# Kernel tuning notes

Hardware: AMD Instinct MI355X
Metric: run time of the kernel (lower is better)

The kernel has to match this reference:

```python
import jax, jax.numpy as jnp
import numpy as np

DIM = 64
HALF = DIM // 2
K = 8
B = 3.0
HID = 256
N = 65536
MIN_BW = 1e-3
MIN_BH = 1e-3
MIN_D = 1e-3


def _mlp(x, w0, b0, w1, b1, w2, b2):
    h = jnp.tanh(x @ w0 + b0)
    h = jnp.tanh(h @ w1 + b1)
    return h @ w2 + b2


def _unconstrained_rqs(x, uW, uH, uD, tail_bound):
    # x: [N, d]; uW, uH: [N, d, K]; uD: [N, d, K-1]
    # Faithful to Durkan/Karpathy unconstrained_RQS (forward, inverse=False).
    left, right, bottom, top = -tail_bound, tail_bound, -tail_bound, tail_bound
    inside = (x >= -tail_bound) & (x <= tail_bound)

    const = float(np.log(np.exp(1.0 - MIN_D) - 1.0))
    uD = jnp.pad(uD, ((0, 0), (0, 0), (1, 1)), constant_values=const)  # [N,d,K+1]

    widths = jax.nn.softmax(uW, axis=-1)
    widths = MIN_BW + (1.0 - MIN_BW * K) * widths
    cumw = jnp.cumsum(widths, axis=-1)
    cumw = jnp.pad(cumw, ((0, 0), (0, 0), (1, 0)))
    cumw = (right - left) * cumw + left
    cumw = cumw.at[..., 0].set(left).at[..., -1].set(right)
    widths = cumw[..., 1:] - cumw[..., :-1]

    derivs = MIN_D + jax.nn.softplus(uD)  # [N,d,K+1]

    heights = jax.nn.softmax(uH, axis=-1)
    heights = MIN_BH + (1.0 - MIN_BH * K) * heights
    cumh = jnp.cumsum(heights, axis=-1)
    cumh = jnp.pad(cumh, ((0, 0), (0, 0), (1, 0)))
    cumh = (top - bottom) * cumh + bottom
    cumh = cumh.at[..., 0].set(bottom).at[..., -1].set(top)
    heights = cumh[..., 1:] - cumh[..., :-1]

    # searchsorted: sum(x >= bin_locations) - 1, with eps on the last edge
    xin = jnp.clip(x, left, right)  # safe values for the outside-interval lanes
    locs = cumw.at[..., -1].add(1e-6)
    bin_idx = jnp.sum(xin[..., None] >= locs, axis=-1) - 1
    bin_idx = jnp.clip(bin_idx, 0, K - 1)

    def g(a):
        return jnp.take_along_axis(a, bin_idx[..., None], axis=-1)[..., 0]

    in_cumw = g(cumw)
    in_w = g(widths)
    in_cumh = g(cumh)
    in_h = g(heights)
    in_delta = g(heights / widths)
    in_d = g(derivs)
    in_d1 = g(derivs[..., 1:])

    theta = (xin - in_cumw) / in_w
    tt = theta * (1.0 - theta)
    numer = in_h * (in_delta * theta * theta + in_d * tt)
    denom = in_delta + (in_d + in_d1 - 2.0 * in_delta) * tt
    out = in_cumh + numer / denom
    dnum = in_delta * in_delta * (in_d1 * theta * theta + 2.0 * in_delta * tt + in_d * (1.0 - theta) ** 2)
    lad = jnp.log(dnum) - 2.0 * jnp.log(denom)

    out = jnp.where(inside, out, x)
    lad = jnp.where(inside, lad, 0.0)
    return out, lad


def _coupling_params(out):
    # out: [N, HALF, 3K-1] -> W, H (softmax * 2B), D (softplus)
    W = out[..., :K]
    H = out[..., K:2 * K]
    D = out[..., 2 * K:]
    W = 2.0 * B * jax.nn.softmax(W, axis=-1)
    H = 2.0 * B * jax.nn.softmax(H, axis=-1)
    D = jax.nn.softplus(D)
    return W, H, D


def setup_inputs() -> dict:
    key = jax.random.key(0)
    ks = jax.random.split(key, 7)
    s = 0.05
    inp = {"x": jax.random.normal(ks[0], (N, DIM), dtype=jnp.float32)}
    out_dim = (3 * K - 1) * HALF
    for i, name in enumerate(["f1", "f2"]):
        kk = jax.random.split(ks[1 + i], 3)
        inp[f"{name}_w0"] = s * jax.random.normal(kk[0], (HALF, HID), dtype=jnp.float32)
        inp[f"{name}_b0"] = jnp.zeros((HID,), dtype=jnp.float32)
        inp[f"{name}_w1"] = s * jax.random.normal(kk[1], (HID, HID), dtype=jnp.float32)
        inp[f"{name}_b1"] = jnp.zeros((HID,), dtype=jnp.float32)
        inp[f"{name}_w2"] = s * jax.random.normal(kk[2], (HID, out_dim), dtype=jnp.float32)
        inp[f"{name}_b2"] = jnp.zeros((out_dim,), dtype=jnp.float32)
    return inp


def reference(x, f1_w0, f1_b0, f1_w1, f1_b1, f1_w2, f1_b2,
              f2_w0, f2_b0, f2_w1, f2_b1, f2_w2, f2_b2):
    lower, upper = x[:, :HALF], x[:, HALF:]

    out = _mlp(lower, f1_w0, f1_b0, f1_w1, f1_b1, f1_w2, f1_b2).reshape(-1, HALF, 3 * K - 1)
    W, H, D = _coupling_params(out)
    upper, ld = _unconstrained_rqs(upper, W, H, D, B)
    log_det = jnp.sum(ld, axis=1)

    out = _mlp(upper, f2_w0, f2_b0, f2_w1, f2_b1, f2_w2, f2_b2).reshape(-1, HALF, 3 * K - 1)
    W, H, D = _coupling_params(out)
    lower, ld = _unconstrained_rqs(lower, W, H, D, B)
    log_det = log_det + jnp.sum(ld, axis=1)

    return jnp.concatenate([lower, upper], axis=1), log_det
```

## Files before the change

### kernel.cpp

```cpp
#include <hip/hip_runtime.h>

#define NHALF 32
#define NDIM  64
#define NHID  256
#define NPAR  736

typedef unsigned short u16;
typedef unsigned int   u32;
typedef __attribute__((ext_vector_type(8))) short short8;
typedef __attribute__((ext_vector_type(4))) float f32x4;

__device__ __forceinline__ float bf2f(u16 h){ return __uint_as_float(((u32)h) << 16); }
__device__ __forceinline__ u16 f2bf(float f){
  u32 u = __float_as_uint(f);
  u += 0x7FFFu + ((u >> 16) & 1u);
  return (u16)(u >> 16);
}
__device__ __forceinline__ float frcp(float x){ return __builtin_amdgcn_rcpf(x); }
__device__ __forceinline__ float tanh_fast(float x){
  x = fminf(15.f, fmaxf(-15.f, x));
  float e = __expf(2.f * x);
  return 1.f - 2.f * frcp(e + 1.f);
}

__device__ __forceinline__ int hoff(int row, int col){
  return row * 264 + (col ^ (((row >> 2) & 3) << 3));
}

template<int XCOL>
__global__ __launch_bounds__(256, 2)
void mlp_fused(const float* __restrict__ X,
               const u16* __restrict__ w0t,
               const u16* __restrict__ w1t,
               const u16* __restrict__ w2t,
               const float* __restrict__ b0, const float* __restrict__ b1,
               const float* __restrict__ b2,
               u16* __restrict__ pr)
{
  __shared__ __align__(16) u16 hb[128 * 264];
  const int t = threadIdx.x, lane = t & 63, w = t >> 6;
  const int lm = lane & 15, lk = lane >> 4;
  const int row0 = blockIdx.x * 128;
  const int cb = w * 64;

  f32x4 acc[8][4];
  const f32x4 zf = (f32x4){0.f, 0.f, 0.f, 0.f};

  {
    short8 a[8];
    #pragma unroll
    for (int mf = 0; mf < 8; mf++){
      const float* xp = X + (size_t)(row0 + mf * 16 + lm) * NDIM + XCOL + lk * 8;
      float4 v0 = *(const float4*)xp;
      float4 v1 = *(const float4*)(xp + 4);
      u16 tmp[8];
      tmp[0] = f2bf(v0.x); tmp[1] = f2bf(v0.y); tmp[2] = f2bf(v0.z); tmp[3] = f2bf(v0.w);
      tmp[4] = f2bf(v1.x); tmp[5] = f2bf(v1.y); tmp[6] = f2bf(v1.z); tmp[7] = f2bf(v1.w);
      a[mf] = *(const short8*)tmp;
    }
    #pragma unroll
    for (int nf = 0; nf < 4; nf++){
      short8 b = *(const short8*)(w0t + (size_t)(cb + nf * 16 + lm) * 32 + lk * 8);
      #pragma unroll
      for (int mf = 0; mf < 8; mf++)
        acc[mf][nf] = __builtin_amdgcn_mfma_f32_16x16x32_bf16(a[mf], b, zf, 0, 0, 0);
    }
    #pragma unroll
    for (int nf = 0; nf < 4; nf++){
      int col = cb + nf * 16 + lm;
      float bs = b0[col];
      #pragma unroll
      for (int mf = 0; mf < 8; mf++)
        #pragma unroll
        for (int r = 0; r < 4; r++)
          hb[hoff(mf * 16 + lk * 4 + r, col)] = f2bf(tanh_fast(acc[mf][nf][r] + bs));
    }
  }
  __syncthreads();

  #pragma unroll
  for (int mf = 0; mf < 8; mf++)
    #pragma unroll
    for (int nf = 0; nf < 4; nf++) acc[mf][nf] = zf;
  for (int ks = 0; ks < 8; ks++){
    short8 av[8], bv[4];
    #pragma unroll
    for (int mf = 0; mf < 8; mf++)
      av[mf] = *(const short8*)(hb + hoff(mf * 16 + lm, ks * 32 + lk * 8));
    #pragma unroll
    for (int nf = 0; nf < 4; nf++)
      bv[nf] = *(const short8*)(w1t + (size_t)(cb + nf * 16 + lm) * 256 + ks * 32 + lk * 8);
    #pragma unroll
    for (int mf = 0; mf < 8; mf++)
      #pragma unroll
      for (int nf = 0; nf < 4; nf++)
        acc[mf][nf] = __builtin_amdgcn_mfma_f32_16x16x32_bf16(av[mf], bv[nf], acc[mf][nf], 0, 0, 0);
  }
  __syncthreads();
  {
    #pragma unroll
    for (int nf = 0; nf < 4; nf++){
      int col = cb + nf * 16 + lm;
      float bs = b1[col];
      #pragma unroll
      for (int mf = 0; mf < 8; mf++)
        #pragma unroll
        for (int r = 0; r < 4; r++)
          hb[hoff(mf * 16 + lk * 4 + r, col)] = f2bf(tanh_fast(acc[mf][nf][r] + bs));
    }
  }
  __syncthreads();

  #pragma unroll 1
  for (int p = 0; p < 3; p++){
    const int cb2 = p * 256 + w * 64;
    #pragma unroll
    for (int mf = 0; mf < 8; mf++)
      #pragma unroll
      for (int nf = 0; nf < 4; nf++) acc[mf][nf] = zf;
    for (int ks = 0; ks < 8; ks++){
      short8 av[8], bv[4];
      #pragma unroll
      for (int mf = 0; mf < 8; mf++)
        av[mf] = *(const short8*)(hb + hoff(mf * 16 + lm, ks * 32 + lk * 8));
      #pragma unroll
      for (int nf = 0; nf < 4; nf++)
        bv[nf] = *(const short8*)(w2t + (size_t)(cb2 + nf * 16 + lm) * 256 + ks * 32 + lk * 8);
      #pragma unroll
      for (int mf = 0; mf < 8; mf++)
        #pragma unroll
        for (int nf = 0; nf < 4; nf++)
          acc[mf][nf] = __builtin_amdgcn_mfma_f32_16x16x32_bf16(av[mf], bv[nf], acc[mf][nf], 0, 0, 0);
    }
    #pragma unroll
    for (int nf = 0; nf < 4; nf++){
      int col = cb2 + nf * 16 + lm;
      if (col < NPAR){
        float bs = b2[col];
        #pragma unroll
        for (int mf = 0; mf < 8; mf++)
          #pragma unroll
          for (int r = 0; r < 4; r++)
            pr[(size_t)(row0 + mf * 16 + lk * 4 + r) * NPAR + col] = f2bf(acc[mf][nf][r] + bs);
      }
    }
  }
}

__global__ __launch_bounds__(256)
void wconv3_k(const float* __restrict__ W0, const float* __restrict__ W1,
              const float* __restrict__ W2,
              u16* __restrict__ w0t, u16* __restrict__ w1t, u16* __restrict__ w2t){
  int tid = blockIdx.x * 256 + threadIdx.x;
  if (tid < 8192){
    int n = tid >> 5, k = tid & 31;
    w0t[tid] = f2bf(W0[(size_t)k * 256 + n]);
  } else if (tid < 73728){
    int id = tid - 8192; int n = id >> 8, k = id & 255;
    w1t[id] = f2bf(W1[(size_t)k * 256 + n]);
  } else if (tid < 270336){
    int id = tid - 73728; int n = id >> 8, k = id & 255;
    w2t[id] = (n < 736) ? f2bf(W2[(size_t)k * 736 + n]) : (u16)0;
  }
}

template<int PHASE>
__global__ __launch_bounds__(256)
void spline_k(const float* __restrict__ x,
              const u16* __restrict__ params,
              float* __restrict__ out,
              float* __restrict__ ldp,
              float* __restrict__ ldout,
              int xcol)
{
  __shared__ u16 pb[8 * NPAR];
  const int t = threadIdx.x;
  const int s0 = blockIdx.x * 8;

  {
    const uint4* src = (const uint4*)(params + (size_t)s0 * NPAR);
    uint4* dst = (uint4*)pb;
    dst[t]       = src[t];
    dst[256 + t] = src[256 + t];
    if (t < 224) dst[512 + t] = src[512 + t];
  }
  __syncthreads();

  const int si = t >> 5, d = t & 31;
  const int s = s0 + si;
  const u16* pp = pb + si * NPAR + d * 23;
  float p[23];
  #pragma unroll
  for (int e = 0; e < 23; e++) p[e] = bf2f(pp[e]);

  float W6[8], H6[8];
  {
    float m = p[0];
    #pragma unroll
    for (int i = 1; i < 8; i++) m = fmaxf(m, p[i]);
    float sm = 0.f;
    #pragma unroll
    for (int i = 0; i < 8; i++){ W6[i] = __expf(p[i] - m); sm += W6[i]; }
    float r = 6.f * frcp(sm);
    #pragma unroll
    for (int i = 0; i < 8; i++) W6[i] *= r;
  }
  {
    float m = p[8];
    #pragma unroll
    for (int i = 1; i < 8; i++) m = fmaxf(m, p[8 + i]);
    float sm = 0.f;
    #pragma unroll
    for (int i = 0; i < 8; i++){ H6[i] = __expf(p[8 + i] - m); sm += H6[i]; }
    float r = 6.f * frcp(sm);
    #pragma unroll
    for (int i = 0; i < 8; i++) H6[i] *= r;
  }

  float wd[8], cumw[9];
  {
    float sm = 0.f;
    #pragma unroll
    for (int i = 0; i < 8; i++){ wd[i] = __expf(W6[i]); sm += wd[i]; }
    float r = 0.992f * frcp(sm);
    #pragma unroll
    for (int i = 0; i < 8; i++) wd[i] = 0.001f + wd[i] * r;
  }
  cumw[0] = -3.f;
  { float run = 0.f;
    #pragma unroll
    for (int i = 0; i < 8; i++){ run += wd[i]; cumw[i + 1] = 6.f * run - 3.f; } }
  cumw[8] = 3.f;
  #pragma unroll
  for (int i = 0; i < 8; i++) wd[i] = cumw[i + 1] - cumw[i];

  float hg[8], cumh[9];
  {
    float sm = 0.f;
    #pragma unroll
    for (int i = 0; i < 8; i++){ hg[i] = __expf(H6[i]); sm += hg[i]; }
    float r = 0.992f * frcp(sm);
    #pragma unroll
    for (int i = 0; i < 8; i++) hg[i] = 0.001f + hg[i] * r;
  }
  cumh[0] = -3.f;
  { float run = 0.f;
    #pragma unroll
    for (int i = 0; i < 8; i++){ run += hg[i]; cumh[i + 1] = 6.f * run - 3.f; } }
  cumh[8] = 3.f;
  #pragma unroll
  for (int i = 0; i < 8; i++) hg[i] = cumh[i + 1] - cumh[i];

  float dv[9];
  dv[0] = 1.f; dv[8] = 1.f;
  #pragma unroll
  for (int j = 0; j < 7; j++){
    float xx  = p[16 + j];
    float z   = __expf(-fabsf(xx));
    float sel = (xx >= 0.f) ? z : 1.f;
    dv[j + 1] = 0.001f + fmaxf(xx, 0.f) + __logf(1.f + z + sel);
  }

  const float xv  = x[(size_t)s * NDIM + xcol + d];
  const float xin = fminf(3.f, fmaxf(-3.f, xv));

  int b = 0;
  #pragma unroll
  for (int j = 1; j < 8; j++) b += (xin >= cumw[j]) ? 1 : 0;

  float in_cw = 0.f, in_w = 0.f, in_ch = 0.f, in_h = 0.f, in_d = 0.f, in_d1 = 0.f;
  #pragma unroll
  for (int j = 0; j < 8; j++){
    if (j == b){ in_cw = cumw[j]; in_w = wd[j]; in_ch = cumh[j];
                 in_h = hg[j];  in_d = dv[j]; in_d1 = dv[j + 1]; }
  }

  float rw    = frcp(in_w);
  float th    = (xin - in_cw) * rw;
  float tt    = th * (1.f - th);
  float delta = in_h * rw;
  float numer = in_h * (delta * th * th + in_d * tt);
  float denom = delta + (in_d + in_d1 - 2.f * delta) * tt;
  float rden  = frcp(denom);
  float outv  = in_ch + numer * rden;
  float omt   = 1.f - th;
  float dnum  = delta * delta * (in_d1 * th * th + 2.f * delta * tt + in_d * omt * omt);
  float lad   = __logf(dnum * rden * rden);

  bool inside = (xv >= -3.f) && (xv <= 3.f);
  outv = inside ? outv : xv;
  lad  = inside ? lad  : 0.f;

  out[(size_t)s * NDIM + xcol + d] = outv;

  float v = lad;
  #pragma unroll
  for (int mm = 1; mm < 32; mm <<= 1) v += __shfl_xor(v, mm, 64);
  if (d == 0){
    if (PHASE == 0) ldp[s] = v;
    else            ldout[s] = ldp[s] + v;
  }
}

extern "C" void kernel_launch(void* const* d_in, const int* in_sizes, int n_in,
                              void* d_out, int out_size, void* d_ws, size_t ws_size,
                              hipStream_t stream)
{
  const float* x    = (const float*)d_in[0];
  const float* f1w0 = (const float*)d_in[1];
  const float* f1b0 = (const float*)d_in[2];
  const float* f1w1 = (const float*)d_in[3];
  const float* f1b1 = (const float*)d_in[4];
  const float* f1w2 = (const float*)d_in[5];
  const float* f1b2 = (const float*)d_in[6];
  const float* f2w0 = (const float*)d_in[7];
  const float* f2b0 = (const float*)d_in[8];
  const float* f2w1 = (const float*)d_in[9];
  const float* f2b1 = (const float*)d_in[10];
  const float* f2w2 = (const float*)d_in[11];
  const float* f2b2 = (const float*)d_in[12];

  const int N = in_sizes[0] / NDIM;
  float* out = (float*)d_out;
  float* ldout = out + (size_t)N * NDIM;

  u16* pr = (u16*)d_ws;
  float* ld1 = (float*)(pr + (size_t)N * NPAR);
  u16* w0t = (u16*)(ld1 + N);
  u16* w1t = w0t + 256 * 32;
  u16* w2t = w1t + 256 * 256;

  dim3 blk(256);
  dim3 gm(N / 128);
  dim3 gw(1056);
  dim3 gs(N / 8);

  wconv3_k<<<gw, blk, 0, stream>>>(f1w0, f1w1, f1w2, w0t, w1t, w2t);
  mlp_fused<0><<<gm, blk, 0, stream>>>(x, w0t, w1t, w2t, f1b0, f1b1, f1b2, pr);
  spline_k<0><<<gs, blk, 0, stream>>>(x, pr, out, ld1, ldout, NHALF);

  wconv3_k<<<gw, blk, 0, stream>>>(f2w0, f2w1, f2w2, w0t, w1t, w2t);
  mlp_fused<NHALF><<<gm, blk, 0, stream>>>(out, w0t, w1t, w2t, f2b0, f2b1, f2b2, pr);
  spline_k<1><<<gs, blk, 0, stream>>>(x, pr, out, ld1, ldout, 0);
}
```

Baseline: 287.4 us.

## Fuse spline evaluation into MLP kernel epilogue, drop separate spline launches

Spline evaluation now runs at the end of the MLP kernel: after the last layer writes bf16 parameters to the global workspace, a __syncthreads is followed by a loop over the block's 128 rows that re-reads those parameters and applies the RQS transform. This removes two kernel launches. The parameters still go through global memory, now reread per thread with strided u16 loads instead of being staged through LDS. It relies on the block's own global writes being visible after __syncthreads, and the spline work runs at the MLP kernel's lower occupancy with a serial 16-step loop.

```diff
diff --git a/kernel.cpp b/kernel.cpp
--- a/kernel.cpp
+++ b/kernel.cpp
@@ -27,15 +27,19 @@
   return row * 264 + (col ^ (((row >> 2) & 3) << 3));
 }
 
-template<int XCOL>
+template<int XMLP, int XSPL, int PHASE>
 __global__ __launch_bounds__(256, 2)
-void mlp_fused(const float* __restrict__ X,
-               const u16* __restrict__ w0t,
-               const u16* __restrict__ w1t,
-               const u16* __restrict__ w2t,
-               const float* __restrict__ b0, const float* __restrict__ b1,
-               const float* __restrict__ b2,
-               u16* __restrict__ pr)
+void mlp_spline(const float* __restrict__ Xm,
+                const float* __restrict__ Xo,
+                const u16* __restrict__ w0t,
+                const u16* __restrict__ w1t,
+                const u16* __restrict__ w2t,
+                const float* __restrict__ b0, const float* __restrict__ b1,
+                const float* __restrict__ b2,
+                u16* __restrict__ pr,
+                float* __restrict__ out,
+                float* __restrict__ ldp,
+                float* __restrict__ ldout)
 {
   __shared__ __align__(16) u16 hb[128 * 264];
   const int t = threadIdx.x, lane = t & 63, w = t >> 6;
@@ -50,7 +54,7 @@
     short8 a[8];
     #pragma unroll
     for (int mf = 0; mf < 8; mf++){
-      const float* xp = X + (size_t)(row0 + mf * 16 + lm) * NDIM + XCOL + lk * 8;
+      const float* xp = Xm + (size_t)(row0 + mf * 16 + lm) * NDIM + XMLP + lk * 8;
       float4 v0 = *(const float4*)xp;
       float4 v1 = *(const float4*)(xp + 4);
       u16 tmp[8];
@@ -143,6 +147,126 @@
           for (int r = 0; r < 4; r++)
             pr[(size_t)(row0 + mf * 16 + lk * 4 + r) * NPAR + col] = f2bf(acc[mf][nf][r] + bs);
       }
+    }
+  }
+  __syncthreads();
+
+  const int d  = t & 31;
+  const int sg = t >> 5;
+  #pragma unroll 1
+  for (int it = 0; it < 16; it++){
+    const int s = row0 + it * 8 + sg;
+    const u16* pp = pr + (size_t)s * NPAR + d * 23;
+    float p[23];
+    #pragma unroll
+    for (int e = 0; e < 23; e++) p[e] = bf2f(pp[e]);
+
+    float W6[8], H6[8];
+    {
+      float m = p[0];
+      #pragma unroll
+      for (int i = 1; i < 8; i++) m = fmaxf(m, p[i]);
+      float sm = 0.f;
+      #pragma unroll
+      for (int i = 0; i < 8; i++){ W6[i] = __expf(p[i] - m); sm += W6[i]; }
+      float r = 6.f * frcp(sm);
+      #pragma unroll
+      for (int i = 0; i < 8; i++) W6[i] *= r;
+    }
+    {
+      float m = p[8];
+      #pragma unroll
+      for (int i = 1; i < 8; i++) m = fmaxf(m, p[8 + i]);
+      float sm = 0.f;
+      #pragma unroll
+      for (int i = 0; i < 8; i++){ H6[i] = __expf(p[8 + i] - m); sm += H6[i]; }
+      float r = 6.f * frcp(sm);
+      #pragma unroll
+      for (int i = 0; i < 8; i++) H6[i] *= r;
+    }
+
+    float wd[8], cumw[9];
+    {
+      float sm = 0.f;
+      #pragma unroll
+      for (int i = 0; i < 8; i++){ wd[i] = __expf(W6[i]); sm += wd[i]; }
+      float r = 0.992f * frcp(sm);
+      #pragma unroll
+      for (int i = 0; i < 8; i++) wd[i] = 0.001f + wd[i] * r;
+    }
+    cumw[0] = -3.f;
+    { float run = 0.f;
+      #pragma unroll
+      for (int i = 0; i < 8; i++){ run += wd[i]; cumw[i + 1] = 6.f * run - 3.f; } }
+    cumw[8] = 3.f;
+    #pragma unroll
+    for (int i = 0; i < 8; i++) wd[i] = cumw[i + 1] - cumw[i];
+
+    float hg[8], cumh[9];
+    {
+      float sm = 0.f;
+      #pragma unroll
+      for (int i = 0; i < 8; i++){ hg[i] = __expf(H6[i]); sm += hg[i]; }
+      float r = 0.992f * frcp(sm);
+      #pragma unroll
+      for (int i = 0; i < 8; i++) hg[i] = 0.001f + hg[i] * r;
+    }
+    cumh[0] = -3.f;
+    { float run = 0.f;
+      #pragma unroll
+      for (int i = 0; i < 8; i++){ run += hg[i]; cumh[i + 1] = 6.f * run - 3.f; } }
+    cumh[8] = 3.f;
+    #pragma unroll
+    for (int i = 0; i < 8; i++) hg[i] = cumh[i + 1] - cumh[i];
+
+    float dv[9];
+    dv[0] = 1.f; dv[8] = 1.f;
+    #pragma unroll
+    for (int j = 0; j < 7; j++){
+      float xx  = p[16 + j];
+      float z   = __expf(-fabsf(xx));
+      float sel = (xx >= 0.f) ? z : 1.f;
+      dv[j + 1] = 0.001f + fmaxf(xx, 0.f) + __logf(1.f + z + sel);
+    }
+
+    const float xv  = Xo[(size_t)s * NDIM + XSPL + d];
+    const float xin = fminf(3.f, fmaxf(-3.f, xv));
+
+    int b = 0;
+    #pragma unroll
+    for (int j = 1; j < 8; j++) b += (xin >= cumw[j]) ? 1 : 0;
+
+    float in_cw = 0.f, in_w = 0.f, in_ch = 0.f, in_h = 0.f, in_d = 0.f, in_d1 = 0.f;
+    #pragma unroll
+    for (int j = 0; j < 8; j++){
+      if (j == b){ in_cw = cumw[j]; in_w = wd[j]; in_ch = cumh[j];
+                   in_h = hg[j];  in_d = dv[j]; in_d1 = dv[j + 1]; }
+    }
+
+    float rw    = frcp(in_w);
+    float th    = (xin - in_cw) * rw;
+    float tt    = th * (1.f - th);
+    float delta = in_h * rw;
+    float numer = in_h * (delta * th * th + in_d * tt);
+    float denom = delta + (in_d + in_d1 - 2.f * delta) * tt;
+    float rden  = frcp(denom);
+    float outv  = in_ch + numer * rden;
+    float omt   = 1.f - th;
+    float dnum  = delta * delta * (in_d1 * th * th + 2.f * delta * tt + in_d * omt * omt);
+    float lad   = __logf(dnum * rden * rden);
+
+    bool inside = (xv >= -3.f) && (xv <= 3.f);
+    outv = inside ? outv : xv;
+    lad  = inside ? lad  : 0.f;
+
+    out[(size_t)s * NDIM + XSPL + d] = outv;
+
+    float v = lad;
+    #pragma unroll
+    for (int mm = 1; mm < 32; mm <<= 1) v += __shfl_xor(v, mm, 64);
+    if (d == 0){
+      if (PHASE == 0) ldp[s] = v;
+      else            ldout[s] = ldp[s] + v;
     }
   }
 }
@@ -161,144 +285,6 @@
   } else if (tid < 270336){
     int id = tid - 73728; int n = id >> 8, k = id & 255;
     w2t[id] = (n < 736) ? f2bf(W2[(size_t)k * 736 + n]) : (u16)0;
-  }
-}
-
-template<int PHASE>
-__global__ __launch_bounds__(256)
-void spline_k(const float* __restrict__ x,
-              const u16* __restrict__ params,
-              float* __restrict__ out,
-              float* __restrict__ ldp,
-              float* __restrict__ ldout,
-              int xcol)
-{
-  __shared__ u16 pb[8 * NPAR];
-  const int t = threadIdx.x;
-  const int s0 = blockIdx.x * 8;
-
-  {
-    const uint4* src = (const uint4*)(params + (size_t)s0 * NPAR);
-    uint4* dst = (uint4*)pb;
-    dst[t]       = src[t];
-    dst[256 + t] = src[256 + t];
-    if (t < 224) dst[512 + t] = src[512 + t];
-  }
-  __syncthreads();
-
-  const int si = t >> 5, d = t & 31;
-  const int s = s0 + si;
-  const u16* pp = pb + si * NPAR + d * 23;
-  float p[23];
-  #pragma unroll
-  for (int e = 0; e < 23; e++) p[e] = bf2f(pp[e]);
-
-  float W6[8], H6[8];
-  {
-    float m = p[0];
-    #pragma unroll
-    for (int i = 1; i < 8; i++) m = fmaxf(m, p[i]);
-    float sm = 0.f;
-    #pragma unroll
-    for (int i = 0; i < 8; i++){ W6[i] = __expf(p[i] - m); sm += W6[i]; }
-    float r = 6.f * frcp(sm);
-    #pragma unroll
-    for (int i = 0; i < 8; i++) W6[i] *= r;
-  }
-  {
-    float m = p[8];
-    #pragma unroll
-    for (int i = 1; i < 8; i++) m = fmaxf(m, p[8 + i]);
-    float sm = 0.f;
-    #pragma unroll
-    for (int i = 0; i < 8; i++){ H6[i] = __expf(p[8 + i] - m); sm += H6[i]; }
-    float r = 6.f * frcp(sm);
-    #pragma unroll
-    for (int i = 0; i < 8; i++) H6[i] *= r;
-  }
-
-  float wd[8], cumw[9];
-  {
-    float sm = 0.f;
-    #pragma unroll
-    for (int i = 0; i < 8; i++){ wd[i] = __expf(W6[i]); sm += wd[i]; }
-    float r = 0.992f * frcp(sm);
-    #pragma unroll
-    for (int i = 0; i < 8; i++) wd[i] = 0.001f + wd[i] * r;
-  }
-  cumw[0] = -3.f;
-  { float run = 0.f;
-    #pragma unroll
-    for (int i = 0; i < 8; i++){ run += wd[i]; cumw[i + 1] = 6.f * run - 3.f; } }
-  cumw[8] = 3.f;
-  #pragma unroll
-  for (int i = 0; i < 8; i++) wd[i] = cumw[i + 1] - cumw[i];
-
-  float hg[8], cumh[9];
-  {
-    float sm = 0.f;
-    #pragma unroll
-    for (int i = 0; i < 8; i++){ hg[i] = __expf(H6[i]); sm += hg[i]; }
-    float r = 0.992f * frcp(sm);
-    #pragma unroll
-    for (int i = 0; i < 8; i++) hg[i] = 0.001f + hg[i] * r;
-  }
-  cumh[0] = -3.f;
-  { float run = 0.f;
-    #pragma unroll
-    for (int i = 0; i < 8; i++){ run += hg[i]; cumh[i + 1] = 6.f * run - 3.f; } }
-  cumh[8] = 3.f;
-  #pragma unroll
-  for (int i = 0; i < 8; i++) hg[i] = cumh[i + 1] - cumh[i];
-
-  float dv[9];
-  dv[0] = 1.f; dv[8] = 1.f;
-  #pragma unroll
-  for (int j = 0; j < 7; j++){
-    float xx  = p[16 + j];
-    float z   = __expf(-fabsf(xx));
-    float sel = (xx >= 0.f) ? z : 1.f;
-    dv[j + 1] = 0.001f + fmaxf(xx, 0.f) + __logf(1.f + z + sel);
-  }
-
-  const float xv  = x[(size_t)s * NDIM + xcol + d];
-  const float xin = fminf(3.f, fmaxf(-3.f, xv));
-
-  int b = 0;
-  #pragma unroll
-  for (int j = 1; j < 8; j++) b += (xin >= cumw[j]) ? 1 : 0;
-
-  float in_cw = 0.f, in_w = 0.f, in_ch = 0.f, in_h = 0.f, in_d = 0.f, in_d1 = 0.f;
-  #pragma unroll
-  for (int j = 0; j < 8; j++){
-    if (j == b){ in_cw = cumw[j]; in_w = wd[j]; in_ch = cumh[j];
-                 in_h = hg[j];  in_d = dv[j]; in_d1 = dv[j + 1]; }
-  }
-
-  float rw    = frcp(in_w);
-  float th    = (xin - in_cw) * rw;
-  float tt    = th * (1.f - th);
-  float delta = in_h * rw;
-  float numer = in_h * (delta * th * th + in_d * tt);
-  float denom = delta + (in_d + in_d1 - 2.f * delta) * tt;
-  float rden  = frcp(denom);
-  float outv  = in_ch + numer * rden;
-  float omt   = 1.f - th;
-  float dnum  = delta * delta * (in_d1 * th * th + 2.f * delta * tt + in_d * omt * omt);
-  float lad   = __logf(dnum * rden * rden);
-
-  bool inside = (xv >= -3.f) && (xv <= 3.f);
-  outv = inside ? outv : xv;
-  lad  = inside ? lad  : 0.f;
-
-  out[(size_t)s * NDIM + xcol + d] = outv;
-
-  float v = lad;
-  #pragma unroll
-  for (int mm = 1; mm < 32; mm <<= 1) v += __shfl_xor(v, mm, 64);
-  if (d == 0){
-    if (PHASE == 0) ldp[s] = v;
-    else            ldout[s] = ldp[s] + v;
   }
 }
 
@@ -333,13 +319,14 @@
   dim3 blk(256);
   dim3 gm(N / 128);
   dim3 gw(1056);
-  dim3 gs(N / 8);
 
   wconv3_k<<<gw, blk, 0, stream>>>(f1w0, f1w1, f1w2, w0t, w1t, w2t);
-  mlp_fused<0><<<gm, blk, 0, stream>>>(x, w0t, w1t, w2t, f1b0, f1b1, f1b2, pr);
-  spline_k<0><<<gs, blk, 0, stream>>>(x, pr, out, ld1, ldout, NHALF);
+  mlp_spline<0, NHALF, 0><<<gm, blk, 0, stream>>>(x, x, w0t, w1t, w2t,
+                                                  f1b0, f1b1, f1b2,
+                                                  pr, out, ld1, ldout);
 
   wconv3_k<<<gw, blk, 0, stream>>>(f2w0, f2w1, f2w2, w0t, w1t, w2t);
-  mlp_fused<NHALF><<<gm, blk, 0, stream>>>(out, w0t, w1t, w2t, f2b0, f2b1, f2b2, pr);
-  spline_k<1><<<gs, blk, 0, stream>>>(x, pr, out, ld1, ldout, 0);
-}
+  mlp_spline<NHALF, 0, 1><<<gm, blk, 0, stream>>>(out, x, w0t, w1t, w2t,
+                                                  f2b0, f2b1, f2b2,
+                                                  pr, out, ld1, ldout);
+}
```

New measurement: 338.5 us. 1.18x slower.
